# Performance work log

Hardware: AMD Instinct MI355X
Metric: run time of the kernel (lower is better)

The kernel has to match this reference:

```python
import jax, jax.numpy as jnp
import numpy as np

EPS = 1e-5

def _layernorm(x, gamma, beta, axes):
    mean = jnp.mean(x, axis=axes, keepdims=True)
    var = jnp.var(x, axis=axes, keepdims=True)
    return (x - mean) * jax.lax.rsqrt(var + EPS) * gamma + beta

def setup_inputs() -> dict:
    key = jax.random.key(0)
    ks = jax.random.split(key, 14)
    B, N1, N2, D1, D2 = 128, 32, 32, 23, 13
    E, H, F = 72, 256, 128
    N = N1 + N2
    s = 0.05
    return {
        "x_a": jax.random.normal(ks[0], (B, N1, D1), jnp.float32),
        "x_b": jax.random.normal(ks[1], (B, N2, D2), jnp.float32),
        "W_a": jax.random.normal(ks[2], (D1, E), jnp.float32) * s,
        "b_a": jnp.zeros((E,), jnp.float32),
        "W_b": jax.random.normal(ks[3], (D2, E), jnp.float32) * s,
        "b_b": jnp.zeros((E,), jnp.float32),
        "ln0_g": jnp.ones((N, E), jnp.float32),
        "ln0_b": jnp.zeros((N, E), jnp.float32),
        "W_g": jax.random.normal(ks[4], (2 * E, H), jnp.float32) * s,
        "b_g": jnp.zeros((H,), jnp.float32),
        "lng_g": jnp.ones((H,), jnp.float32),
        "lng_b": jnp.zeros((H,), jnp.float32),
        "W_f": jax.random.normal(ks[5], (H, F), jnp.float32) * s,
        "b_f": jnp.zeros((F,), jnp.float32),
    }

def reference(x_a, x_b, W_a, b_a, W_b, b_b, ln0_g, ln0_b,
              W_g, b_g, lng_g, lng_b, W_f, b_f):
    # SplitEmbedding: per-group linear embed, concat along entity dim
    a = jnp.concatenate([x_a @ W_a + b_a, x_b @ W_b + b_b], axis=-2)  # [B, N, E]
    # LayerNorm over last two dims (num_entities, embed_dim) jointly
    a = _layernorm(a, ln0_g, ln0_b, axes=(-2, -1))
    B, N, E = a.shape
    # ij(): aij[b, i, j] = concat(a[b, i], a[b, j])  -> [B, N, N, 2E]
    ai = jnp.broadcast_to(a[:, :, None, :], (B, N, N, E))
    aj = jnp.broadcast_to(a[:, None, :, :], (B, N, N, E))
    aij = jnp.concatenate([ai, aj], axis=-1)
    # g: Linear(2E, H) + ELU, then LayerNorm(H)
    g = jax.nn.elu(aij @ W_g + b_g)  # [B, N, N, H]
    g = _layernorm(g, lng_g, lng_b, axes=(-1,))
    # sum over both pairwise dims
    s = jnp.sum(g, axis=(-3, -2))  # [B, H]
    # f: Linear(H, F) + ELU
    return jax.nn.elu(s @ W_f + b_f)  # [B, F]
```

## Files before the change

kernel.cpp:

```cpp
#include <hip/hip_runtime.h>
#include <hip/hip_bf16.h>

#define EPS 1e-5f
#define LOG2E 1.44269504088896f
#define LN2   0.69314718055995f

typedef float v2f __attribute__((ext_vector_type(2)));

#define OFF_ABAR 0
#define OFF_U    589824
#define OFF_V    2686976
#define OFF_PART 4784128

__device__ __forceinline__ float elu(float z) {
    return z > 0.f ? z : __expf(z) - 1.f;
}

__device__ __forceinline__ v2f vmin0(v2f a) {
#if __has_builtin(__builtin_elementwise_min)
    return __builtin_elementwise_min(a, (v2f){0.f, 0.f});
#else
    return (v2f){fminf(a.x, 0.f), fminf(a.y, 0.f)};
#endif
}
__device__ __forceinline__ v2f vmax0(v2f a) {
#if __has_builtin(__builtin_elementwise_max)
    return __builtin_elementwise_max(a, (v2f){0.f, 0.f});
#else
    return (v2f){fmaxf(a.x, 0.f), fmaxf(a.y, 0.f)};
#endif
}

template <int CTRL>
__device__ __forceinline__ float ror_add(float x) {
    int xi = __builtin_bit_cast(int, x);
    int yi = __builtin_amdgcn_update_dpp(xi, xi, CTRL, 0xF, 0xF, false);
    return x + __builtin_bit_cast(float, yi);
}
__device__ __forceinline__ float row16_sum(float x) {
    x = ror_add<0x128>(x);
    x = ror_add<0x124>(x);
    x = ror_add<0x122>(x);
    x = ror_add<0x121>(x);
    return x;
}

__global__ __launch_bounds__(256) void k_embed_ln0(
    const float* __restrict__ xa, const float* __restrict__ xb,
    const float* __restrict__ Wa, const float* __restrict__ ba,
    const float* __restrict__ Wb, const float* __restrict__ bb,
    const float* __restrict__ g0, const float* __restrict__ b0,
    float* __restrict__ abar) {
    int b = blockIdx.x;
    int tid = threadIdx.x;
    __shared__ float S[3888];
    float* s_xa = S;
    float* s_xb = S + 736;
    float* s_Wa = S + 1152;
    float* s_Wb = S + 2808;
    float* s_ba = S + 3744;
    float* s_bb = S + 3816;
    for (int k = tid; k < 736;  k += 256) s_xa[k] = xa[b * 736 + k];
    for (int k = tid; k < 416;  k += 256) s_xb[k] = xb[b * 416 + k];
    for (int k = tid; k < 1656; k += 256) s_Wa[k] = Wa[k];
    for (int k = tid; k < 936;  k += 256) s_Wb[k] = Wb[k];
    if (tid < 72) { s_ba[tid] = ba[tid]; s_bb[tid] = bb[tid]; }
    __syncthreads();

    float vals[18];
    float s1 = 0.f, s2 = 0.f;
    #pragma unroll
    for (int m = 0; m < 18; ++m) {
        int k = tid + 256 * m;
        int e = k % 72;
        int n = k / 72;
        float acc;
        if (n < 32) {
            acc = s_ba[e];
            const float* x = s_xa + n * 23;
            #pragma unroll
            for (int d = 0; d < 23; ++d) acc = fmaf(x[d], s_Wa[d * 72 + e], acc);
        } else {
            acc = s_bb[e];
            const float* x = s_xb + (n - 32) * 13;
            #pragma unroll
            for (int d = 0; d < 13; ++d) acc = fmaf(x[d], s_Wb[d * 72 + e], acc);
        }
        vals[m] = acc;
        s1 += acc;
        s2 = fmaf(acc, acc, s2);
    }
    #pragma unroll
    for (int off = 32; off >= 1; off >>= 1) {
        s1 += __shfl_xor(s1, off, 64);
        s2 += __shfl_xor(s2, off, 64);
    }
    __shared__ float r1[4], r2[4];
    int w = tid >> 6;
    if ((tid & 63) == 0) { r1[w] = s1; r2[w] = s2; }
    __syncthreads();
    float t1 = r1[0] + r1[1] + r1[2] + r1[3];
    float t2 = r2[0] + r2[1] + r2[2] + r2[3];
    float mean = t1 * (1.f / 4608.f);
    float var  = fmaf(-mean, mean, t2 * (1.f / 4608.f));
    float rsq  = rsqrtf(var + EPS);
    float* ab = abar + b * 4608;
    #pragma unroll
    for (int m = 0; m < 18; ++m) {
        int k = tid + 256 * m;
        ab[k] = fmaf((vals[m] - mean) * rsq, g0[k], b0[k]);
    }
}

__global__ __launch_bounds__(256) void k_uv(
    const float* __restrict__ abar, const float* __restrict__ Wg,
    const float* __restrict__ bg,
    float* __restrict__ U, float* __restrict__ V) {
    int blk = blockIdx.x;
    int b = blk >> 3;
    int q = blk & 7;
    int h = threadIdx.x;
    __shared__ float sa[72 * 8];
    const float* src = abar + (b * 64 + q * 8) * 72;
    for (int k = threadIdx.x; k < 72 * 8; k += 256) {
        int e = k >> 3, n = k & 7;
        sa[k] = src[n * 72 + e];
    }
    __syncthreads();
    float u[8], v[8];
    #pragma unroll
    for (int n = 0; n < 8; ++n) { u[n] = 0.f; v[n] = 0.f; }
    #pragma unroll 6
    for (int e = 0; e < 72; ++e) {
        float wu = Wg[e * 256 + h];
        float wv = Wg[(72 + e) * 256 + h];
        const float4* sp = (const float4*)&sa[e * 8];
        #pragma unroll
        for (int n4 = 0; n4 < 2; ++n4) {
            float4 s4 = sp[n4];
            u[n4*4+0] = fmaf(s4.x, wu, u[n4*4+0]); v[n4*4+0] = fmaf(s4.x, wv, v[n4*4+0]);
            u[n4*4+1] = fmaf(s4.y, wu, u[n4*4+1]); v[n4*4+1] = fmaf(s4.y, wv, v[n4*4+1]);
            u[n4*4+2] = fmaf(s4.z, wu, u[n4*4+2]); v[n4*4+2] = fmaf(s4.z, wv, v[n4*4+2]);
            u[n4*4+3] = fmaf(s4.w, wu, u[n4*4+3]); v[n4*4+3] = fmaf(s4.w, wv, v[n4*4+3]);
        }
    }
    float bgh = bg[h];
    int base = (b * 64 + q * 8) * 256 + h;
    #pragma unroll
    for (int n = 0; n < 8; ++n) {
        U[base + n * 256] = (u[n] + bgh) * LOG2E;
        V[base + n * 256] = v[n] * LOG2E;
    }
}

__global__ __launch_bounds__(256) void k_pair(
    const float* __restrict__ U, const float* __restrict__ V,
    float* __restrict__ part) {
    int blk = (blockIdx.x & 7) * 256 + (blockIdx.x >> 3);
    int b  = blk >> 4;
    int iq = blk & 15;
    int t  = threadIdx.x;
    int j16 = t >> 4;
    int hc  = t & 15;

    __shared__ float Sc[16 * 256];

    v2f u2[4][8];
    #pragma unroll
    for (int i = 0; i < 4; ++i) {
        const float* Ur = U + (size_t)(b * 64 + iq * 4 + i) * 256;
        #pragma unroll
        for (int c = 0; c < 4; ++c) {
            float4 x = *(const float4*)&Ur[hc * 4 + 64 * c];
            u2[i][2*c]   = (v2f){x.x, x.y};
            u2[i][2*c+1] = (v2f){x.z, x.w};
        }
    }

    #pragma unroll
    for (int jq = 0; jq < 4; ++jq) {
        const float* Vrow = V + (size_t)(b * 64 + jq * 16 + j16) * 256;
        v2f v[8];
        #pragma unroll
        for (int c = 0; c < 4; ++c) {
            float4 v4 = *(const float4*)&Vrow[hc * 4 + 64 * c];
            v[2*c]   = (v2f){v4.x, v4.y};
            v[2*c+1] = (v2f){v4.z, v4.w};
        }

        v2f acc[8];
        #pragma unroll
        for (int k = 0; k < 8; ++k) acc[k] = (v2f){0.f, 0.f};
        float macc = 0.f;

        v2f t2[4][8];
        float s1h[4], s2h[4];
        #pragma unroll
        for (int i = 0; i < 4; ++i) {
            v2f s1v = (v2f){0.f, 0.f};
            v2f s2v = (v2f){0.f, 0.f};
            #pragma unroll
            for (int c = 0; c < 8; ++c) {
                v2f z  = u2[i][c] + v[c];
                v2f mn = vmin0(z);
                v2f mx = vmax0(z);
                v2f ex;
                ex.x = __builtin_amdgcn_exp2f(mn.x);
                ex.y = __builtin_amdgcn_exp2f(mn.y);
                v2f tt = mx * (v2f){LN2, LN2} + ex;
                t2[i][c] = tt;
                s1v += tt;
                s2v = tt * tt + s2v;
            }
            s1h[i] = s1v.x + s1v.y;
            s2h[i] = s2v.x + s2v.y;
        }
        #pragma unroll
        for (int i = 0; i < 4; ++i) {
            s1h[i] = row16_sum(s1h[i]);
            s2h[i] = row16_sum(s2h[i]);
        }
        float rsq4[4];
        #pragma unroll
        for (int i = 0; i < 4; ++i) {
            float mu  = s1h[i] * (1.f / 256.f);
            float var = fmaf(-mu, mu, s2h[i] * (1.f / 256.f));
            rsq4[i] = rsqrtf(var + EPS);
            macc += mu * rsq4[i];
        }
        #pragma unroll
        for (int i = 0; i < 4; ++i) {
            v2f r2 = (v2f){rsq4[i], rsq4[i]};
            #pragma unroll
            for (int k = 0; k < 8; ++k) acc[k] = t2[i][k] * r2 + acc[k];
        }
        v2f m2 = (v2f){macc, macc};
        #pragma unroll
        for (int k = 0; k < 8; ++k) acc[k] -= m2;

        if (jq == 0) {
            #pragma unroll
            for (int c = 0; c < 4; ++c)
                *(float4*)&Sc[j16 * 256 + hc * 4 + 64 * c] =
                    make_float4(acc[2*c].x, acc[2*c].y, acc[2*c+1].x, acc[2*c+1].y);
        } else {
            #pragma unroll
            for (int c = 0; c < 4; ++c) {
                float* p = &Sc[j16 * 256 + hc * 4 + 64 * c];
                float4 old = *(const float4*)p;
                *(float4*)p = make_float4(old.x + acc[2*c].x, old.y + acc[2*c].y,
                                          old.z + acc[2*c+1].x, old.w + acc[2*c+1].y);
            }
        }
    }

    __syncthreads();
    float r = 0.f;
    #pragma unroll
    for (int q = 0; q < 16; ++q) r += Sc[q * 256 + t];
    part[(size_t)blk * 256 + t] = r;
}

__global__ __launch_bounds__(512) void k_out(
    const float* __restrict__ part,
    const float* __restrict__ lgg, const float* __restrict__ lgb,
    const float* __restrict__ Wf,  const float* __restrict__ bfb,
    float* __restrict__ out) {
    int b = blockIdx.x;
    int t = threadIdx.x;
    __shared__ float sh[256];
    __shared__ float ps[512];
    {
        int h = t & 255, pg = t >> 8;
        float s = 0.f;
        #pragma unroll
        for (int p = 0; p < 8; ++p)
            s += part[(size_t)(b * 16 + pg * 8 + p) * 256 + h];
        ps[t] = s;
    }
    __syncthreads();
    if (t < 256) sh[t] = fmaf(lgg[t], ps[t] + ps[t + 256], 4096.f * lgb[t]);
    __syncthreads();
    {
        int f = t & 127, hq = t >> 7;
        float acc = 0.f;
        #pragma unroll 8
        for (int h = hq * 64; h < hq * 64 + 64; ++h)
            acc = fmaf(sh[h], Wf[h * 128 + f], acc);
        ps[t] = acc;
    }
    __syncthreads();
    if (t < 128) {
        float r = ps[t] + ps[t + 128] + ps[t + 256] + ps[t + 384] + bfb[t];
        out[b * 128 + t] = r > 0.f ? r : __expf(r) - 1.f;
    }
}

extern "C" void kernel_launch(void* const* d_in, const int* in_sizes, int n_in,
                              void* d_out, int out_size, void* d_ws, size_t ws_size,
                              hipStream_t stream) {
    const float* xa  = (const float*)d_in[0];
    const float* xb  = (const float*)d_in[1];
    const float* Wa  = (const float*)d_in[2];
    const float* ba  = (const float*)d_in[3];
    const float* Wb  = (const float*)d_in[4];
    const float* bb  = (const float*)d_in[5];
    const float* g0  = (const float*)d_in[6];
    const float* b0  = (const float*)d_in[7];
    const float* Wg  = (const float*)d_in[8];
    const float* bg  = (const float*)d_in[9];
    const float* lgg = (const float*)d_in[10];
    const float* lgb = (const float*)d_in[11];
    const float* Wf  = (const float*)d_in[12];
    const float* bfb = (const float*)d_in[13];
    float* out = (float*)d_out;

    float* ws   = (float*)d_ws;
    float* abar = ws + OFF_ABAR;
    float* U    = ws + OFF_U;
    float* V    = ws + OFF_V;
    float* part = ws + OFF_PART;

    k_embed_ln0<<<128, 256, 0, stream>>>(xa, xb, Wa, ba, Wb, bb, g0, b0, abar);
    k_uv<<<1024, 256, 0, stream>>>(abar, Wg, bg, U, V);
    k_pair<<<2048, 256, 0, stream>>>(U, V, part);
    k_out<<<128, 512, 0, stream>>>(part, lgg, lgb, Wf, bfb, out);
}
```

Measured before the change: 150.1 us.

## Fuse embedding+LayerNorm with U/V projection into one kernel

Merges the embed/LN0 kernel and the U/V projection kernel into a single kernel with two blocks per batch. Each block recomputes the full-sample embedding and LN statistics, then writes its 32 normalized rows transposed into shared memory and projects them to U and V. This removes one launch and the round trip of the normalized activations through global memory. In exchange it duplicates the embedding work, cuts the projection grid from 1024 to 256 blocks, and raises per-thread register use with 64 accumulators.

```diff
diff --git a/kernel.cpp b/kernel.cpp
--- a/kernel.cpp
+++ b/kernel.cpp
@@ -7,7 +7,6 @@
 
 typedef float v2f __attribute__((ext_vector_type(2)));
 
-#define OFF_ABAR 0
 #define OFF_U    589824
 #define OFF_V    2686976
 #define OFF_PART 4784128
@@ -45,15 +44,21 @@
     return x;
 }
 
-__global__ __launch_bounds__(256) void k_embed_ln0(
+__global__ __launch_bounds__(256) void k_embed_uv(
     const float* __restrict__ xa, const float* __restrict__ xb,
     const float* __restrict__ Wa, const float* __restrict__ ba,
     const float* __restrict__ Wb, const float* __restrict__ bb,
     const float* __restrict__ g0, const float* __restrict__ b0,
-    float* __restrict__ abar) {
-    int b = blockIdx.x;
-    int tid = threadIdx.x;
+    const float* __restrict__ Wg, const float* __restrict__ bg,
+    float* __restrict__ U, float* __restrict__ V) {
+    int blk = blockIdx.x;
+    int b    = blk >> 1;
+    int n0   = (blk & 1) * 32;
+    int tid  = threadIdx.x;
+
     __shared__ float S[3888];
+    __shared__ float sa[72 * 32];
+    __shared__ float r1[4], r2[4];
     float* s_xa = S;
     float* s_xb = S + 736;
     float* s_Wa = S + 1152;
@@ -95,7 +100,6 @@
         s1 += __shfl_xor(s1, off, 64);
         s2 += __shfl_xor(s2, off, 64);
     }
-    __shared__ float r1[4], r2[4];
     int w = tid >> 6;
     if ((tid & 63) == 0) { r1[w] = s1; r2[w] = s2; }
     __syncthreads();
@@ -104,52 +108,52 @@
     float mean = t1 * (1.f / 4608.f);
     float var  = fmaf(-mean, mean, t2 * (1.f / 4608.f));
     float rsq  = rsqrtf(var + EPS);
-    float* ab = abar + b * 4608;
+
     #pragma unroll
     for (int m = 0; m < 18; ++m) {
         int k = tid + 256 * m;
-        ab[k] = fmaf((vals[m] - mean) * rsq, g0[k], b0[k]);
-    }
-}
-
-__global__ __launch_bounds__(256) void k_uv(
-    const float* __restrict__ abar, const float* __restrict__ Wg,
-    const float* __restrict__ bg,
-    float* __restrict__ U, float* __restrict__ V) {
-    int blk = blockIdx.x;
-    int b = blk >> 3;
-    int q = blk & 7;
-    int h = threadIdx.x;
-    __shared__ float sa[72 * 8];
-    const float* src = abar + (b * 64 + q * 8) * 72;
-    for (int k = threadIdx.x; k < 72 * 8; k += 256) {
-        int e = k >> 3, n = k & 7;
-        sa[k] = src[n * 72 + e];
-    }
-    __syncthreads();
-    float u[8], v[8];
-    #pragma unroll
-    for (int n = 0; n < 8; ++n) { u[n] = 0.f; v[n] = 0.f; }
-    #pragma unroll 6
+        int dn = k / 72 - n0;
+        if ((unsigned)dn < 32u) {
+            int e = k % 72;
+            sa[e * 32 + dn] = fmaf((vals[m] - mean) * rsq, g0[k], b0[k]);
+        }
+    }
+    __syncthreads();
+
+    int h = tid;
+    float u[4][8], v[4][8];
+    #pragma unroll
+    for (int q = 0; q < 4; ++q)
+        #pragma unroll
+        for (int n = 0; n < 8; ++n) { u[q][n] = 0.f; v[q][n] = 0.f; }
+    #pragma unroll 2
     for (int e = 0; e < 72; ++e) {
         float wu = Wg[e * 256 + h];
         float wv = Wg[(72 + e) * 256 + h];
-        const float4* sp = (const float4*)&sa[e * 8];
-        #pragma unroll
-        for (int n4 = 0; n4 < 2; ++n4) {
-            float4 s4 = sp[n4];
-            u[n4*4+0] = fmaf(s4.x, wu, u[n4*4+0]); v[n4*4+0] = fmaf(s4.x, wv, v[n4*4+0]);
-            u[n4*4+1] = fmaf(s4.y, wu, u[n4*4+1]); v[n4*4+1] = fmaf(s4.y, wv, v[n4*4+1]);
-            u[n4*4+2] = fmaf(s4.z, wu, u[n4*4+2]); v[n4*4+2] = fmaf(s4.z, wv, v[n4*4+2]);
-            u[n4*4+3] = fmaf(s4.w, wu, u[n4*4+3]); v[n4*4+3] = fmaf(s4.w, wv, v[n4*4+3]);
+        const float4* sp = (const float4*)&sa[e * 32];
+        #pragma unroll
+        for (int q = 0; q < 4; ++q) {
+            float4 sA = sp[2 * q];
+            float4 sB = sp[2 * q + 1];
+            u[q][0] = fmaf(sA.x, wu, u[q][0]); v[q][0] = fmaf(sA.x, wv, v[q][0]);
+            u[q][1] = fmaf(sA.y, wu, u[q][1]); v[q][1] = fmaf(sA.y, wv, v[q][1]);
+            u[q][2] = fmaf(sA.z, wu, u[q][2]); v[q][2] = fmaf(sA.z, wv, v[q][2]);
+            u[q][3] = fmaf(sA.w, wu, u[q][3]); v[q][3] = fmaf(sA.w, wv, v[q][3]);
+            u[q][4] = fmaf(sB.x, wu, u[q][4]); v[q][4] = fmaf(sB.x, wv, v[q][4]);
+            u[q][5] = fmaf(sB.y, wu, u[q][5]); v[q][5] = fmaf(sB.y, wv, v[q][5]);
+            u[q][6] = fmaf(sB.z, wu, u[q][6]); v[q][6] = fmaf(sB.z, wv, v[q][6]);
+            u[q][7] = fmaf(sB.w, wu, u[q][7]); v[q][7] = fmaf(sB.w, wv, v[q][7]);
         }
     }
     float bgh = bg[h];
-    int base = (b * 64 + q * 8) * 256 + h;
-    #pragma unroll
-    for (int n = 0; n < 8; ++n) {
-        U[base + n * 256] = (u[n] + bgh) * LOG2E;
-        V[base + n * 256] = v[n] * LOG2E;
+    #pragma unroll
+    for (int q = 0; q < 4; ++q) {
+        int base = (b * 64 + n0 + q * 8) * 256 + h;
+        #pragma unroll
+        for (int n = 0; n < 8; ++n) {
+            U[base + n * 256] = (u[q][n] + bgh) * LOG2E;
+            V[base + n * 256] = v[q][n] * LOG2E;
+        }
     }
 }
 
@@ -316,13 +320,12 @@
     float* out = (float*)d_out;
 
     float* ws   = (float*)d_ws;
-    float* abar = ws + OFF_ABAR;
     float* U    = ws + OFF_U;
     float* V    = ws + OFF_V;
     float* part = ws + OFF_PART;
 
-    k_embed_ln0<<<128, 256, 0, stream>>>(xa, xb, Wa, ba, Wb, bb, g0, b0, abar);
-    k_uv<<<1024, 256, 0, stream>>>(abar, Wg, bg, U, V);
+    k_embed_uv<<<256, 256, 0, stream>>>(xa, xb, Wa, ba, Wb, bb, g0, b0,
+                                        Wg, bg, U, V);
     k_pair<<<2048, 256, 0, stream>>>(U, V, part);
     k_out<<<128, 512, 0, stream>>>(part, lgg, lgb, Wf, bfb, out);
 }
```

After: 157.4 us. +4.9%, slower.
